# Optimization experiments

Hardware: AMD Instinct MI355X
Metric: run time of the kernel (lower is better)

## Reference

```python
import jax, jax.numpy as jnp
import numpy as np

NEG_SLOPE = 0.2  # PyG GATConv leaky_relu negative_slope
EPS = 1e-16      # PyG softmax denominator epsilon


def _add_self_loops(edge_index, edge_attr, N):
    # PyG add_self_loops with fill_value='mean': loop attr = mean of incoming edge attrs
    src, dst = edge_index[0], edge_index[1]
    ones = jnp.ones((src.shape[0],), edge_attr.dtype)
    cnt = jax.ops.segment_sum(ones, dst, num_segments=N)
    loop_attr = jax.ops.segment_sum(edge_attr, dst, num_segments=N) / jnp.maximum(cnt, 1.0)[:, None]
    loops = jnp.arange(N, dtype=src.dtype)
    return (jnp.concatenate([src, loops]),
            jnp.concatenate([dst, loops]),
            jnp.concatenate([edge_attr, loop_attr], axis=0))


def _gat_conv(x, src, dst, ea, W, We, att_src, att_dst, att_edge, bias, heads, out_ch):
    N = x.shape[0]
    h = (x @ W).reshape(N, heads, out_ch)              # [N,H,C]
    a_src = (h * att_src).sum(-1)                      # [N,H]
    a_dst = (h * att_dst).sum(-1)                      # [N,H]
    e = (ea @ We).reshape(-1, heads, out_ch)           # [E,H,C]
    a_edge = (e * att_edge).sum(-1)                    # [E,H]
    alpha = jax.nn.leaky_relu(a_src[src] + a_dst[dst] + a_edge, NEG_SLOPE)
    amax = jax.ops.segment_max(alpha, dst, num_segments=N)
    alpha = jnp.exp(alpha - amax[dst])
    denom = jax.ops.segment_sum(alpha, dst, num_segments=N)
    alpha = alpha / (denom[dst] + EPS)
    out = jax.ops.segment_sum(h[src] * alpha[..., None], dst, num_segments=N)  # [N,H,C]
    return out.mean(axis=1) + bias                     # concat=False -> mean over heads


def setup_inputs() -> dict:
    key = jax.random.key(0)
    ks = jax.random.split(key, 16)
    N, E, F_in, HID, OUT, H = 50000, 800000, 64, 16, 8, 8
    s = 0.1
    return {
        "x": jax.random.normal(ks[0], (N, F_in), jnp.float32),
        "edge_index": jax.random.randint(ks[1], (2, E), 0, N, dtype=jnp.int64),
        "edge_attr": jax.random.uniform(ks[2], (E, 1), jnp.float32),
        "W1": jax.random.normal(ks[3], (F_in, H * HID), jnp.float32) * s,
        "We1": jax.random.normal(ks[4], (1, H * HID), jnp.float32) * s,
        "att_src1": jax.random.normal(ks[5], (H, HID), jnp.float32) * s,
        "att_dst1": jax.random.normal(ks[6], (H, HID), jnp.float32) * s,
        "att_edge1": jax.random.normal(ks[7], (H, HID), jnp.float32) * s,
        "b1": jnp.zeros((HID,), jnp.float32),
        "W2": jax.random.normal(ks[8], (HID, OUT), jnp.float32) * s,
        "We2": jax.random.normal(ks[9], (1, OUT), jnp.float32) * s,
        "att_src2": jax.random.normal(ks[10], (1, OUT), jnp.float32) * s,
        "att_dst2": jax.random.normal(ks[11], (1, OUT), jnp.float32) * s,
        "att_edge2": jax.random.normal(ks[12], (1, OUT), jnp.float32) * s,
        "b2": jnp.zeros((OUT,), jnp.float32),
    }


def reference(x, edge_index, edge_attr, W1, We1, att_src1, att_dst1, att_edge1, b1,
              W2, We2, att_src2, att_dst2, att_edge2, b2):
    N = x.shape[0]
    src, dst, ea = _add_self_loops(edge_index, edge_attr, N)
    h = jax.nn.relu(_gat_conv(x, src, dst, ea, W1, We1, att_src1, att_dst1, att_edge1, b1, 8, 16))
    # dropout is identity in eval mode
    return _gat_conv(h, src, dst, ea, W2, We2, att_src2, att_dst2, att_edge2, b2, 1, 8)
```

## Files before the change

### kernel.cpp

```cpp
#include <hip/hip_runtime.h>
#include <hip/hip_fp16.h>
#include <math.h>

#define EPS 1e-16f
#define LOG2E 1.44269504088896340736f

typedef _Float16 half8 __attribute__((ext_vector_type(8)));
typedef float floatx4 __attribute__((ext_vector_type(4)));

#define RNG 4
#define NRR 16384
#define RB  64


__global__ __launch_bounds__(256) void k_hist(int E, int CH, const int* __restrict__ ei,
                                              int* __restrict__ H, int* __restrict__ rank) {
    int r = blockIdx.x / RB, b = blockIdx.x % RB;
    __shared__ int hist[NRR];
    for (int i = threadIdx.x; i < NRR; i += 256) hist[i] = 0;
    __syncthreads();
    int lo = b * CH, hi = min(E, (b + 1) * CH);
    int rlo = r << 14;
#pragma unroll 4
    for (int e = lo + threadIdx.x; e < hi; e += 256) {
        int d = ei[E + e];
        int dr = d - rlo;
        if ((unsigned)dr < NRR) rank[e] = atomicAdd(&hist[dr], 1);
    }
    __syncthreads();
    int* Hb = H + (size_t)blockIdx.x * NRR;
    for (int i = threadIdx.x; i < NRR; i += 256) Hb[i] = hist[i];
}

__global__ __launch_bounds__(256) void k_cntscan(int N, int* __restrict__ H,
                                                 int* rowptr, int* bsums) {
    __shared__ int sm[256];
    int t = threadIdx.x;
    int n = blockIdx.x * 256 + t;
    int sum = 0;
    if (n < N) {
        int r = n >> 14, dr = n & (NRR - 1);
        size_t base = ((size_t)(r * RB)) * NRR + dr;
#pragma unroll 8
        for (int b = 0; b < RB; ++b) {
            size_t idx = base + (size_t)b * NRR;
            int v = H[idx];
            H[idx] = sum;
            sum += v;
        }
    }
    int val = (n < N) ? sum : 0;
    sm[t] = val; __syncthreads();
    for (int ofs = 1; ofs < 256; ofs <<= 1) {
        int v = (t >= ofs) ? sm[t - ofs] : 0;
        __syncthreads();
        sm[t] += v;
        __syncthreads();
    }
    if (n < N) rowptr[n] = sm[t] - val;
    if (t == 255) bsums[blockIdx.x] = sm[255];
}

__global__ void k_scan2(int nb, int N, int* bsums, int* rowptr) {
    __shared__ int sm[256];
    int t = threadIdx.x;
    int v = (t < nb) ? bsums[t] : 0;
    sm[t] = v; __syncthreads();
    for (int ofs = 1; ofs < 256; ofs <<= 1) {
        int u = (t >= ofs) ? sm[t - ofs] : 0;
        __syncthreads();
        sm[t] += u;
        __syncthreads();
    }
    if (t < nb) bsums[t] = sm[t] - v;
    if (t == 255) rowptr[N] = sm[255];
}

__global__ void k_scan3(int N, int* rowptr, const int* __restrict__ bsums) {
    int n = blockIdx.x * blockDim.x + threadIdx.x;
    if (n < N) rowptr[n] += bsums[n >> 8];
}


__global__ __launch_bounds__(256) void k_misc(
    int N, int nbX, const float* __restrict__ x, _Float16* __restrict__ xh,
    const float* __restrict__ W1, _Float16* __restrict__ Wpk,
    const float* __restrict__ We1, const float* __restrict__ ae1,
    const float* __restrict__ We2, const float* __restrict__ ae2,
    float* __restrict__ wed) {
    int bid = blockIdx.x;
    if (bid < nbX) {
        int t = bid * 256 + threadIdx.x;
        int row = t >> 3;
        half8 h;
        if (row < N) {
            const float4* pp = (const float4*)(x + (size_t)t * 8);
            float4 f0 = pp[0], f1 = pp[1];
            h[0] = (_Float16)f0.x; h[1] = (_Float16)f0.y; h[2] = (_Float16)f0.z; h[3] = (_Float16)f0.w;
            h[4] = (_Float16)f1.x; h[5] = (_Float16)f1.y; h[6] = (_Float16)f1.z; h[7] = (_Float16)f1.w;
        } else {
#pragma unroll
            for (int i = 0; i < 8; ++i) h[i] = (_Float16)0.0f;
        }
        *(half8*)(xh + (size_t)t * 8) = h;
    } else {
        int t = threadIdx.x;
        for (int i = 0; i < 32; ++i) {
            int idx = i * 256 + t;
            int j  = idx & 7;
            int lq = (idx >> 3) & 63;
            int ks = (idx >> 9) & 1;
            int ct = idx >> 10;
            int k   = ks * 32 + (lq >> 4) * 8 + j;
            int col = ct * 16 + (lq & 15);
            Wpk[idx] = (_Float16)W1[k * 128 + col];
        }
        if (t < 8) {
            float ssum = 0.0f;
            for (int cc = 0; cc < 16; ++cc) ssum += We1[t * 16 + cc] * ae1[t * 16 + cc];
            wed[t] = ssum * LOG2E;
        }
        if (t == 8) {
            float ssum = 0.0f;
            for (int cc = 0; cc < 8; ++cc) ssum += We2[cc] * ae2[cc];
            wed[8] = ssum * LOG2E;
        }
    }
}


#define LDSP 132

__global__ __launch_bounds__(128) void k_scatgemm(
    int E, int CH, int SB, const int* __restrict__ ei, const float* __restrict__ ea,
    const int* __restrict__ rowptr, const int* __restrict__ H, const int* __restrict__ rank,
    int2* __restrict__ rec,
    int N, const _Float16* __restrict__ xh, const _Float16* __restrict__ Wpk,
    const float* __restrict__ att_s, const float* __restrict__ att_d,
    __half* __restrict__ h1, float* __restrict__ asrc, float* __restrict__ adst) {
    __shared__ float hs[2 * 16 * LDSP];
    if ((int)blockIdx.x < SB) {
        int e = blockIdx.x * 128 + threadIdx.x;
        if (e < E) {
            int s = ei[e], d = ei[E + e];
            int r = d >> 14, dr = d & (NRR - 1);
            int b = e / CH;
            int pos = rowptr[d] + H[((size_t)(r * RB + b)) * NRR + dr] + rank[e];
            unsigned long long pk = ((unsigned long long)(unsigned)__float_as_int(ea[e]) << 32)
                                  | (unsigned long long)(unsigned)s;
            __builtin_nontemporal_store(pk, (unsigned long long*)&rec[pos]);
        } else if (e < E + 32) {
            rec[e] = make_int2(0, 0);
        }
        return;
    }
    int blk = blockIdx.x - SB;
    int tid = threadIdx.x;
    int w = tid >> 6, l = tid & 63;
    int row0 = blk * 32 + w * 16;
    int arow = row0 + (l & 15);
    half8 a0 = *(const half8*)(xh + (size_t)arow * 64 + (l >> 4) * 8);
    half8 a1 = *(const half8*)(xh + (size_t)arow * 64 + 32 + (l >> 4) * 8);
    float* base = &hs[w * 16 * LDSP];
    int r0 = (l >> 4) * 4;
#pragma unroll
    for (int ct = 0; ct < 8; ++ct) {
        half8 b0 = *(const half8*)(Wpk + ((ct * 2 + 0) * 64 + l) * 8);
        half8 b1 = *(const half8*)(Wpk + ((ct * 2 + 1) * 64 + l) * 8);
        floatx4 acc = {0.f, 0.f, 0.f, 0.f};
        acc = __builtin_amdgcn_mfma_f32_16x16x32_f16(a0, b0, acc, 0, 0, 0);
        acc = __builtin_amdgcn_mfma_f32_16x16x32_f16(a1, b1, acc, 0, 0, 0);
        int col = ct * 16 + (l & 15);
#pragma unroll
        for (int i = 0; i < 4; ++i)
            base[(r0 + i) * LDSP + col] = acc[i];
    }
    __syncthreads();
    int r = tid >> 2, g = tid & 3;
    int rg = blk * 32 + r;
    if (rg >= N) return;
    float v[32];
    const float* rp = &hs[r * LDSP + g * 32];
#pragma unroll
    for (int j = 0; j < 8; ++j) {
        floatx4 t4 = *(const floatx4*)(rp + j * 4);
        v[j * 4 + 0] = t4[0]; v[j * 4 + 1] = t4[1];
        v[j * 4 + 2] = t4[2]; v[j * 4 + 3] = t4[3];
    }
    float vs0 = 0.f, vs1 = 0.f, vd0 = 0.f, vd1 = 0.f;
    const float4* as4 = (const float4*)(att_s + g * 32);
    const float4* ad4 = (const float4*)(att_d + g * 32);
#pragma unroll
    for (int j = 0; j < 4; ++j) {
        float4 a4 = as4[j], d4 = ad4[j];
        vs0 += v[j*4+0]*a4.x + v[j*4+1]*a4.y + v[j*4+2]*a4.z + v[j*4+3]*a4.w;
        vd0 += v[j*4+0]*d4.x + v[j*4+1]*d4.y + v[j*4+2]*d4.z + v[j*4+3]*d4.w;
    }
#pragma unroll
    for (int j = 4; j < 8; ++j) {
        float4 a4 = as4[j], d4 = ad4[j];
        vs1 += v[j*4+0]*a4.x + v[j*4+1]*a4.y + v[j*4+2]*a4.z + v[j*4+3]*a4.w;
        vd1 += v[j*4+0]*d4.x + v[j*4+1]*d4.y + v[j*4+2]*d4.z + v[j*4+3]*d4.w;
    }
    union { __half h[32]; float4 f4[4]; } u;
#pragma unroll
    for (int i = 0; i < 32; ++i) u.h[i] = __float2half(v[i]);
    float4* hp = (float4*)(h1 + (size_t)rg * 128 + g * 32);
#pragma unroll
    for (int j = 0; j < 4; ++j) hp[j] = u.f4[j];
    asrc[rg * 8 + g * 2]     = vs0 * LOG2E;
    asrc[rg * 8 + g * 2 + 1] = vs1 * LOG2E;
    adst[rg * 8 + g * 2]     = vd0 * LOG2E;
    adst[rg * 8 + g * 2 + 1] = vd1 * LOG2E;
}


__global__ __launch_bounds__(256) void k_agg1(
    int N, const int* __restrict__ rowptr, const int2* __restrict__ rec,
    const float* __restrict__ asrc1, const float* __restrict__ adst1,
    const float* __restrict__ wed,
    const __half* __restrict__ h1v, const float* __restrict__ b1,
    const float* __restrict__ W2, const float* __restrict__ as2w, const float* __restrict__ ad2w,
    float* __restrict__ hh2, float* __restrict__ asrc2, float* __restrict__ adst2) {
    __shared__ __align__(16) float hs[4 * 1088];
    int tid = threadIdx.x;
    int wid = (blockIdx.x * blockDim.x + tid) >> 6;
    if (wid >= N) return;
    int l = tid & 63, w = tid >> 6;
    int eo = l >> 3, hd = l & 7;
    int start = rowptr[wid], end = rowptr[wid + 1];
    int len = end - start;
    float adn = adst1[wid * 8 + hd];
    float wdh = wed[hd];
    const _Float16* h1p = (const _Float16*)h1v;

    float acc[16];
#pragma unroll
    for (int k = 0; k < 16; ++k) acc[k] = 0.f;
    float denom = 0.f, esum = 0.f;
    int e = start + eo;
    int2 rv  = rec[e];
    int2 rn1 = rec[e + 8];
    float av = asrc1[rv.x * 8 + hd];
    int nIt = (len + 7) >> 3;
    for (int it = 0; it < nIt; ++it) {
        const _Float16* hr = h1p + (((size_t)rv.x) << 7) + hd * 16;
        float4 hv0 = *(const float4*)hr;
        float4 hv1 = *(const float4*)(hr + 8);
        int2 rn2 = rec[e + 16];
        float an = asrc1[rn1.x * 8 + hd];
        float wgt = __int_as_float(rv.y);
        float a = av + adn + wgt * wdh;
        a = fmaxf(a, 0.2f * a);
        bool valid = (e < end);
        float p = valid ? exp2f(a) : 0.f;
        esum += valid ? wgt : 0.f;
        denom += p;
        const _Float16* x0 = (const _Float16*)&hv0;
        const _Float16* x1 = (const _Float16*)&hv1;
#pragma unroll
        for (int k = 0; k < 8; ++k) acc[k]     = fmaf(p, (float)x0[k], acc[k]);
#pragma unroll
        for (int k = 0; k < 8; ++k) acc[8 + k] = fmaf(p, (float)x1[k], acc[8 + k]);
        rv = rn1; rn1 = rn2; av = an; e += 8;
    }
    esum += __shfl_xor(esum, 8);
    esum += __shfl_xor(esum, 16);
    esum += __shfl_xor(esum, 32);
    float mean = esum / (float)max(len, 1);
    float aself = asrc1[wid * 8 + hd] + adn + mean * wdh;
    aself = fmaxf(aself, 0.2f * aself);
    float pself = exp2f(aself);
    if (eo == 0) {
        denom += pself;
        const _Float16* hr = h1p + (((size_t)wid) << 7) + hd * 16;
        float4 hv0 = *(const float4*)hr;
        float4 hv1 = *(const float4*)(hr + 8);
        const _Float16* x0 = (const _Float16*)&hv0;
        const _Float16* x1 = (const _Float16*)&hv1;
#pragma unroll
        for (int k = 0; k < 8; ++k) acc[k]     = fmaf(pself, (float)x0[k], acc[k]);
#pragma unroll
        for (int k = 0; k < 8; ++k) acc[8 + k] = fmaf(pself, (float)x1[k], acc[8 + k]);
    }
    denom += __shfl_xor(denom, 8);
    denom += __shfl_xor(denom, 16);
    denom += __shfl_xor(denom, 32);
    float invd = 1.0f / (denom + EPS);
    float* hw = &hs[w * 1088];
#pragma unroll
    for (int k = 0; k < 16; ++k) hw[k * 68 + l] = acc[k] * invd;
    int c = l & 15, qt = l >> 4;
    const floatx4* rp4 = (const floatx4*)&hw[c * 68 + qt * 16];
    floatx4 s0 = rp4[0], s1 = rp4[1], s2 = rp4[2], s3 = rp4[3];
    float v = ((s0[0] + s0[1]) + (s0[2] + s0[3])) + ((s1[0] + s1[1]) + (s1[2] + s1[3]))
            + ((s2[0] + s2[1]) + (s2[2] + s2[3])) + ((s3[0] + s3[1]) + (s3[2] + s3[3]));
    v += __shfl_xor(v, 16);
    v += __shfl_xor(v, 32);
    float t = fmaxf(v * 0.125f + b1[c], 0.f);
    float p0 = t * W2[c * 8 + 2 * qt];
    float p1 = t * W2[c * 8 + 2 * qt + 1];
#pragma unroll
    for (int m = 1; m <= 8; m <<= 1) {
        p0 += __shfl_xor(p0, m);
        p1 += __shfl_xor(p1, m);
    }
    if (c == 0) *(float2*)&hh2[(size_t)wid * 8 + 2 * qt] = make_float2(p0, p1);
    float sd = p0 * as2w[2 * qt] + p1 * as2w[2 * qt + 1];
    float dd = p0 * ad2w[2 * qt] + p1 * ad2w[2 * qt + 1];
    sd += __shfl_xor(sd, 16); sd += __shfl_xor(sd, 32);
    dd += __shfl_xor(dd, 16); dd += __shfl_xor(dd, 32);
    if (l == 0) { asrc2[wid] = sd * LOG2E; adst2[wid] = dd * LOG2E; }
}


__global__ __launch_bounds__(256) void k_agg2(
    int N, const int* __restrict__ rowptr, const int2* __restrict__ rec,
    const float* __restrict__ asrc2, const float* __restrict__ adst2,
    const float* __restrict__ wed,
    const float* __restrict__ hh, const float* __restrict__ b2, float* __restrict__ out) {
    int wid = (blockIdx.x * blockDim.x + threadIdx.x) >> 6;
    if (wid >= N) return;
    int l = threadIdx.x & 63;
    int eo = l >> 3, c = l & 7;
    int start = rowptr[wid], end = rowptr[wid + 1];
    int len = end - start;
    int G = (len + 7) >> 3;
    int nIt = (G + 1) >> 1;
    int startB = start + (nIt << 3);
    int endA = min(startB, end);
    float adn = adst2[wid];
    float w2 = wed[8];

    float acc = 0.0f, denom = 0.0f, esum = 0.0f;
    int eA = start + eo, eB = startB + eo;
    int2 rvA  = rec[eA];
    int2 rnA1 = rec[eA + 8];
    int2 rvB  = rec[eB];
    int2 rnB1 = rec[eB + 8];
    float avA = asrc2[rvA.x];
    float avB = asrc2[rvB.x];
    for (int it = 0; it < nIt; ++it) {
        float hvA = hh[(size_t)rvA.x * 8 + c];
        float hvB = hh[(size_t)rvB.x * 8 + c];
        int2 rnA2 = rec[eA + 16];
        int2 rnB2 = rec[eB + 16];
        float anA = asrc2[rnA1.x];
        float anB = asrc2[rnB1.x];
        float wA = __int_as_float(rvA.y);
        float wB = __int_as_float(rvB.y);
        float aA = avA + adn + wA * w2;
        aA = fmaxf(aA, 0.2f * aA);
        bool vA = (eA < endA);
        float pA = vA ? exp2f(aA) : 0.0f;
        float aB = avB + adn + wB * w2;
        aB = fmaxf(aB, 0.2f * aB);
        bool vB = (eB < end);
        float pB = vB ? exp2f(aB) : 0.0f;
        esum += (vA ? wA : 0.f) + (vB ? wB : 0.f);
        denom += pA + pB;
        acc = fmaf(pA, hvA, fmaf(pB, hvB, acc));
        rvA = rnA1; rnA1 = rnA2; avA = anA; eA += 8;
        rvB = rnB1; rnB1 = rnB2; avB = anB; eB += 8;
    }
    esum += __shfl_xor(esum, 8); esum += __shfl_xor(esum, 16); esum += __shfl_xor(esum, 32);
    float mean = esum / (float)max(len, 1);
    float aself = asrc2[wid] + adn + mean * w2;
    aself = fmaxf(aself, 0.2f * aself);
    float pself = exp2f(aself);
    if (eo == 0) {
        denom += pself;
        acc = fmaf(pself, hh[(size_t)wid * 8 + c], acc);
    }
    acc += __shfl_xor(acc, 8);  acc += __shfl_xor(acc, 16);  acc += __shfl_xor(acc, 32);
    denom += __shfl_xor(denom, 8); denom += __shfl_xor(denom, 16); denom += __shfl_xor(denom, 32);
    if (l < 8) out[(size_t)wid * 8 + l] = acc / (denom + EPS) + b2[l];
}


extern "C" void kernel_launch(void* const* d_in, const int* in_sizes, int n_in,
                              void* d_out, int out_size, void* d_ws, size_t ws_size,
                              hipStream_t stream) {
    const float* x        = (const float*)d_in[0];
    const int*   ei       = (const int*)d_in[1];
    const float* ea       = (const float*)d_in[2];
    const float* W1       = (const float*)d_in[3];
    const float* We1      = (const float*)d_in[4];
    const float* att_src1 = (const float*)d_in[5];
    const float* att_dst1 = (const float*)d_in[6];
    const float* att_edge1= (const float*)d_in[7];
    const float* b1       = (const float*)d_in[8];
    const float* W2       = (const float*)d_in[9];
    const float* We2      = (const float*)d_in[10];
    const float* att_src2 = (const float*)d_in[11];
    const float* att_dst2 = (const float*)d_in[12];
    const float* att_edge2= (const float*)d_in[13];
    const float* b2       = (const float*)d_in[14];
    float* out = (float*)d_out;

    const int N = in_sizes[0] / 64;
    const int E = in_sizes[2];
    const int CH = (E + RB - 1) / RB;
    const int NB64 = (N + 63) / 64;
    const int Mpad = NB64 * 64;
    const int SB = (E + 32 + 127) / 128;
    const int GB = Mpad / 32;

    char* p = (char*)d_ws;
    auto alloc = [&](size_t bytes) { void* r = (void*)p; p += (bytes + 255) & ~(size_t)255; return r; };
    int*   rowptr = (int*)  alloc((size_t)(N + 1) * 4);
    int*   bsums  = (int*)  alloc((size_t)4096 * 4);
    int2*  rec    = (int2*) alloc((size_t)(E + 32) * 8);
    _Float16* Wpk = (_Float16*)alloc((size_t)8192 * 2);
    _Float16* xh  = (_Float16*)alloc((size_t)Mpad * 64 * 2);
    __half* h1    = (__half*)alloc((size_t)Mpad * 128 * 2);
    float* asrc1  = (float*)alloc((size_t)N * 8 * 4);
    float* adst1  = (float*)alloc((size_t)N * 8 * 4);
    float* hh2    = (float*)alloc((size_t)N * 8 * 4);
    float* asrc2  = (float*)alloc((size_t)N * 4);
    float* adst2  = (float*)alloc((size_t)N * 4);
    float* wed    = (float*)alloc(16 * 4);
    int*   rank   = (int*)  alloc((size_t)E * 4);
    int*   H      = (int*)  alloc((size_t)RNG * RB * NRR * 4);

    const int nbN = (N + 255) / 256;
    const int nbX = Mpad / 32;

    hipLaunchKernelGGL(k_misc,     dim3(nbX + 1), dim3(256), 0, stream, N, nbX,
                       x, xh, W1, Wpk, We1, att_edge1, We2, att_edge2, wed);
    hipLaunchKernelGGL(k_hist,     dim3(RNG * RB), dim3(256), 0, stream, E, CH, ei, H, rank);
    hipLaunchKernelGGL(k_cntscan,  dim3(nbN), dim3(256), 0, stream, N, H, rowptr, bsums);
    hipLaunchKernelGGL(k_scan2,    dim3(1), dim3(256), 0, stream, nbN, N, bsums, rowptr);
    hipLaunchKernelGGL(k_scan3,    dim3(nbN), dim3(256), 0, stream, N, rowptr, bsums);
    hipLaunchKernelGGL(k_scatgemm, dim3(SB + GB), dim3(128), 0, stream, E, CH, SB, ei, ea,
                       rowptr, H, rank, rec, N, xh, Wpk, att_src1, att_dst1, h1, asrc1, adst1);
    hipLaunchKernelGGL(k_agg1,     dim3((N + 3) / 4), dim3(256), 0, stream, N, rowptr, rec,
                       asrc1, adst1, wed, h1, b1, W2, att_src2, att_dst2, hh2, asrc2, adst2);
    hipLaunchKernelGGL(k_agg2,     dim3((N + 3) / 4), dim3(256), 0, stream, N, rowptr, rec,
                       asrc2, adst2, wed, hh2, b2, out);
}
```

Before: 137.6 us.

## Fuse histogram with prep kernel, merge scan passes, narrow counts to u16

Merges the x/W conversion kernel with the destination histogram kernel into one launch, and folds the two final scan kernels into a single kernel where each block rescans the block sums. Histogram counts and per-edge ranks are stored as 16-bit values to halve their memory traffic. The agg1 LDS transpose changes to a stride-65 layout with scalar reads instead of padded vector reads. This saves launches and bandwidth, but relies on per-chunk counts fitting in 16 bits and adds redundant scan work per block.

```diff
diff --git a/kernel.cpp b/kernel.cpp
--- a/kernel.cpp
+++ b/kernel.cpp
@@ -13,26 +13,74 @@
 #define RB  64
 
 
-__global__ __launch_bounds__(256) void k_hist(int E, int CH, const int* __restrict__ ei,
-                                              int* __restrict__ H, int* __restrict__ rank) {
-    int r = blockIdx.x / RB, b = blockIdx.x % RB;
+__global__ __launch_bounds__(256) void k_prephist(
+    int E, int CH, const int* __restrict__ ei,
+    unsigned short* __restrict__ H, unsigned short* __restrict__ rank,
+    int N, int nbX, const float* __restrict__ x, _Float16* __restrict__ xh,
+    const float* __restrict__ W1, _Float16* __restrict__ Wpk,
+    const float* __restrict__ We1, const float* __restrict__ ae1,
+    const float* __restrict__ We2, const float* __restrict__ ae2,
+    float* __restrict__ wed) {
     __shared__ int hist[NRR];
-    for (int i = threadIdx.x; i < NRR; i += 256) hist[i] = 0;
-    __syncthreads();
-    int lo = b * CH, hi = min(E, (b + 1) * CH);
-    int rlo = r << 14;
+    int bid = blockIdx.x;
+    if (bid < RNG * RB) {
+        int r = bid / RB, b = bid % RB;
+        for (int i = threadIdx.x; i < NRR; i += 256) hist[i] = 0;
+        __syncthreads();
+        int lo = b * CH, hi = min(E, (b + 1) * CH);
+        int rlo = r << 14;
 #pragma unroll 4
-    for (int e = lo + threadIdx.x; e < hi; e += 256) {
-        int d = ei[E + e];
-        int dr = d - rlo;
-        if ((unsigned)dr < NRR) rank[e] = atomicAdd(&hist[dr], 1);
-    }
-    __syncthreads();
-    int* Hb = H + (size_t)blockIdx.x * NRR;
-    for (int i = threadIdx.x; i < NRR; i += 256) Hb[i] = hist[i];
-}
-
-__global__ __launch_bounds__(256) void k_cntscan(int N, int* __restrict__ H,
+        for (int e = lo + threadIdx.x; e < hi; e += 256) {
+            int d = ei[E + e];
+            int dr = d - rlo;
+            if ((unsigned)dr < NRR) rank[e] = (unsigned short)atomicAdd(&hist[dr], 1);
+        }
+        __syncthreads();
+        unsigned short* Hb = H + (size_t)bid * NRR;
+        for (int i = threadIdx.x; i < NRR; i += 256) Hb[i] = (unsigned short)hist[i];
+        return;
+    }
+    int mb = bid - RNG * RB;
+    if (mb < nbX) {
+        int t = mb * 256 + threadIdx.x;
+        int row = t >> 3;
+        half8 h;
+        if (row < N) {
+            const float4* pp = (const float4*)(x + (size_t)t * 8);
+            float4 f0 = pp[0], f1 = pp[1];
+            h[0] = (_Float16)f0.x; h[1] = (_Float16)f0.y; h[2] = (_Float16)f0.z; h[3] = (_Float16)f0.w;
+            h[4] = (_Float16)f1.x; h[5] = (_Float16)f1.y; h[6] = (_Float16)f1.z; h[7] = (_Float16)f1.w;
+        } else {
+#pragma unroll
+            for (int i = 0; i < 8; ++i) h[i] = (_Float16)0.0f;
+        }
+        *(half8*)(xh + (size_t)t * 8) = h;
+    } else {
+        int t = threadIdx.x;
+        for (int i = 0; i < 32; ++i) {
+            int idx = i * 256 + t;
+            int j  = idx & 7;
+            int lq = (idx >> 3) & 63;
+            int ks = (idx >> 9) & 1;
+            int ct = idx >> 10;
+            int k   = ks * 32 + (lq >> 4) * 8 + j;
+            int col = ct * 16 + (lq & 15);
+            Wpk[idx] = (_Float16)W1[k * 128 + col];
+        }
+        if (t < 8) {
+            float ssum = 0.0f;
+            for (int cc = 0; cc < 16; ++cc) ssum += We1[t * 16 + cc] * ae1[t * 16 + cc];
+            wed[t] = ssum * LOG2E;
+        }
+        if (t == 8) {
+            float ssum = 0.0f;
+            for (int cc = 0; cc < 8; ++cc) ssum += We2[cc] * ae2[cc];
+            wed[8] = ssum * LOG2E;
+        }
+    }
+}
+
+__global__ __launch_bounds__(256) void k_cntscan(int N, unsigned short* __restrict__ H,
                                                  int* rowptr, int* bsums) {
     __shared__ int sm[256];
     int t = threadIdx.x;
@@ -45,7 +93,7 @@
         for (int b = 0; b < RB; ++b) {
             size_t idx = base + (size_t)b * NRR;
             int v = H[idx];
-            H[idx] = sum;
+            H[idx] = (unsigned short)sum;
             sum += v;
         }
     }
@@ -61,71 +109,23 @@
     if (t == 255) bsums[blockIdx.x] = sm[255];
 }
 
-__global__ void k_scan2(int nb, int N, int* bsums, int* rowptr) {
+__global__ __launch_bounds__(256) void k_scanadd(int nb, int N, const int* __restrict__ bsums,
+                                                 int* rowptr) {
     __shared__ int sm[256];
     int t = threadIdx.x;
-    int v = (t < nb) ? bsums[t] : 0;
-    sm[t] = v; __syncthreads();
+    int bid = blockIdx.x;
+    sm[t] = (t < nb) ? bsums[t] : 0;
+    __syncthreads();
     for (int ofs = 1; ofs < 256; ofs <<= 1) {
-        int u = (t >= ofs) ? sm[t - ofs] : 0;
-        __syncthreads();
-        sm[t] += u;
-        __syncthreads();
-    }
-    if (t < nb) bsums[t] = sm[t] - v;
-    if (t == 255) rowptr[N] = sm[255];
-}
-
-__global__ void k_scan3(int N, int* rowptr, const int* __restrict__ bsums) {
-    int n = blockIdx.x * blockDim.x + threadIdx.x;
-    if (n < N) rowptr[n] += bsums[n >> 8];
-}
-
-
-__global__ __launch_bounds__(256) void k_misc(
-    int N, int nbX, const float* __restrict__ x, _Float16* __restrict__ xh,
-    const float* __restrict__ W1, _Float16* __restrict__ Wpk,
-    const float* __restrict__ We1, const float* __restrict__ ae1,
-    const float* __restrict__ We2, const float* __restrict__ ae2,
-    float* __restrict__ wed) {
-    int bid = blockIdx.x;
-    if (bid < nbX) {
-        int t = bid * 256 + threadIdx.x;
-        int row = t >> 3;
-        half8 h;
-        if (row < N) {
-            const float4* pp = (const float4*)(x + (size_t)t * 8);
-            float4 f0 = pp[0], f1 = pp[1];
-            h[0] = (_Float16)f0.x; h[1] = (_Float16)f0.y; h[2] = (_Float16)f0.z; h[3] = (_Float16)f0.w;
-            h[4] = (_Float16)f1.x; h[5] = (_Float16)f1.y; h[6] = (_Float16)f1.z; h[7] = (_Float16)f1.w;
-        } else {
-#pragma unroll
-            for (int i = 0; i < 8; ++i) h[i] = (_Float16)0.0f;
-        }
-        *(half8*)(xh + (size_t)t * 8) = h;
-    } else {
-        int t = threadIdx.x;
-        for (int i = 0; i < 32; ++i) {
-            int idx = i * 256 + t;
-            int j  = idx & 7;
-            int lq = (idx >> 3) & 63;
-            int ks = (idx >> 9) & 1;
-            int ct = idx >> 10;
-            int k   = ks * 32 + (lq >> 4) * 8 + j;
-            int col = ct * 16 + (lq & 15);
-            Wpk[idx] = (_Float16)W1[k * 128 + col];
-        }
-        if (t < 8) {
-            float ssum = 0.0f;
-            for (int cc = 0; cc < 16; ++cc) ssum += We1[t * 16 + cc] * ae1[t * 16 + cc];
-            wed[t] = ssum * LOG2E;
-        }
-        if (t == 8) {
-            float ssum = 0.0f;
-            for (int cc = 0; cc < 8; ++cc) ssum += We2[cc] * ae2[cc];
-            wed[8] = ssum * LOG2E;
-        }
-    }
+        int v = (t >= ofs) ? sm[t - ofs] : 0;
+        __syncthreads();
+        sm[t] += v;
+        __syncthreads();
+    }
+    int prefix = (bid > 0) ? sm[bid - 1] : 0;
+    int n = bid * 256 + t;
+    if (n < N) rowptr[n] += prefix;
+    if (bid == 0 && t == 0) rowptr[N] = sm[nb - 1];
 }
 
 
@@ -133,8 +133,8 @@
 
 __global__ __launch_bounds__(128) void k_scatgemm(
     int E, int CH, int SB, const int* __restrict__ ei, const float* __restrict__ ea,
-    const int* __restrict__ rowptr, const int* __restrict__ H, const int* __restrict__ rank,
-    int2* __restrict__ rec,
+    const int* __restrict__ rowptr, const unsigned short* __restrict__ H,
+    const unsigned short* __restrict__ rank, int2* __restrict__ rec,
     int N, const _Float16* __restrict__ xh, const _Float16* __restrict__ Wpk,
     const float* __restrict__ att_s, const float* __restrict__ att_d,
     __half* __restrict__ h1, float* __restrict__ asrc, float* __restrict__ adst) {
@@ -145,7 +145,7 @@
             int s = ei[e], d = ei[E + e];
             int r = d >> 14, dr = d & (NRR - 1);
             int b = e / CH;
-            int pos = rowptr[d] + H[((size_t)(r * RB + b)) * NRR + dr] + rank[e];
+            int pos = rowptr[d] + (int)H[((size_t)(r * RB + b)) * NRR + dr] + (int)rank[e];
             unsigned long long pk = ((unsigned long long)(unsigned)__float_as_int(ea[e]) << 32)
                                   | (unsigned long long)(unsigned)s;
             __builtin_nontemporal_store(pk, (unsigned long long*)&rec[pos]);
@@ -222,7 +222,7 @@
     const __half* __restrict__ h1v, const float* __restrict__ b1,
     const float* __restrict__ W2, const float* __restrict__ as2w, const float* __restrict__ ad2w,
     float* __restrict__ hh2, float* __restrict__ asrc2, float* __restrict__ adst2) {
-    __shared__ __align__(16) float hs[4 * 1088];
+    __shared__ float hs[4 * 1040];
     int tid = threadIdx.x;
     int wid = (blockIdx.x * blockDim.x + tid) >> 6;
     if (wid >= N) return;
@@ -287,14 +287,14 @@
     denom += __shfl_xor(denom, 16);
     denom += __shfl_xor(denom, 32);
     float invd = 1.0f / (denom + EPS);
-    float* hw = &hs[w * 1088];
-#pragma unroll
-    for (int k = 0; k < 16; ++k) hw[k * 68 + l] = acc[k] * invd;
+    float* hw = &hs[w * 1040];
+#pragma unroll
+    for (int k = 0; k < 16; ++k) hw[k * 65 + l] = acc[k] * invd;
     int c = l & 15, qt = l >> 4;
-    const floatx4* rp4 = (const floatx4*)&hw[c * 68 + qt * 16];
-    floatx4 s0 = rp4[0], s1 = rp4[1], s2 = rp4[2], s3 = rp4[3];
-    float v = ((s0[0] + s0[1]) + (s0[2] + s0[3])) + ((s1[0] + s1[1]) + (s1[2] + s1[3]))
-            + ((s2[0] + s2[1]) + (s2[2] + s2[3])) + ((s3[0] + s3[1]) + (s3[2] + s3[3]));
+    const float* rp = &hw[c * 65 + qt * 16];
+    float v = 0.f;
+#pragma unroll
+    for (int i = 0; i < 16; ++i) v += rp[i];
     v += __shfl_xor(v, 16);
     v += __shfl_xor(v, 32);
     float t = fmaxf(v * 0.125f + b1[c], 0.f);
@@ -420,18 +420,17 @@
     float* asrc2  = (float*)alloc((size_t)N * 4);
     float* adst2  = (float*)alloc((size_t)N * 4);
     float* wed    = (float*)alloc(16 * 4);
-    int*   rank   = (int*)  alloc((size_t)E * 4);
-    int*   H      = (int*)  alloc((size_t)RNG * RB * NRR * 4);
+    unsigned short* rank = (unsigned short*)alloc((size_t)E * 2);
+    unsigned short* H    = (unsigned short*)alloc((size_t)RNG * RB * NRR * 2);
 
     const int nbN = (N + 255) / 256;
     const int nbX = Mpad / 32;
 
-    hipLaunchKernelGGL(k_misc,     dim3(nbX + 1), dim3(256), 0, stream, N, nbX,
-                       x, xh, W1, Wpk, We1, att_edge1, We2, att_edge2, wed);
-    hipLaunchKernelGGL(k_hist,     dim3(RNG * RB), dim3(256), 0, stream, E, CH, ei, H, rank);
+    hipLaunchKernelGGL(k_prephist, dim3(RNG * RB + nbX + 1), dim3(256), 0, stream,
+                       E, CH, ei, H, rank,
+                       N, nbX, x, xh, W1, Wpk, We1, att_edge1, We2, att_edge2, wed);
     hipLaunchKernelGGL(k_cntscan,  dim3(nbN), dim3(256), 0, stream, N, H, rowptr, bsums);
-    hipLaunchKernelGGL(k_scan2,    dim3(1), dim3(256), 0, stream, nbN, N, bsums, rowptr);
-    hipLaunchKernelGGL(k_scan3,    dim3(nbN), dim3(256), 0, stream, N, rowptr, bsums);
+    hipLaunchKernelGGL(k_scanadd,  dim3(nbN), dim3(256), 0, stream, nbN, N, bsums, rowptr);
     hipLaunchKernelGGL(k_scatgemm, dim3(SB + GB), dim3(128), 0, stream, E, CH, SB, ei, ea,
                        rowptr, H, rank, rec, N, xh, Wpk, att_src1, att_dst1, h1, asrc1, adst1);
     hipLaunchKernelGGL(k_agg1,     dim3((N + 3) / 4), dim3(256), 0, stream, N, rowptr, rec,
```

Measured after the change: 128.3 us. 1.07x faster.
